# Optimization experiments

Measured on AMD Instinct MI355X. Metric: run time of the kernel, lower is better.

Reference implementation:

```python
import jax, jax.numpy as jnp
import numpy as np

N_NODES = 50000
N_EDGES = 800000
IN, N1, N2, N3, N4, N5, L, NC = 7, 128, 128, 64, 64, 16, 16, 3


def _gat_params(key, fin, fout, edge_dim=1):
    ks = jax.random.split(key, 6)
    s = 0.1
    return dict(
        W=jax.random.normal(ks[0], (fin, fout), jnp.float32) * s,
        a_src=jax.random.normal(ks[1], (fout,), jnp.float32) * s,
        a_dst=jax.random.normal(ks[2], (fout,), jnp.float32) * s,
        We=jax.random.normal(ks[3], (edge_dim, fout), jnp.float32) * s,
        a_e=jax.random.normal(ks[4], (fout,), jnp.float32) * s,
        b=jax.random.normal(ks[5], (fout,), jnp.float32) * s,
    )


def setup_inputs() -> dict:
    key = jax.random.key(0)
    ks = jax.random.split(key, 16)
    inp = {
        'x1': jax.random.normal(ks[0], (N_NODES, IN), jnp.float32),
        'x2': jax.random.normal(ks[1], (N_NODES, IN), jnp.float32),
        'edge_index1': jax.random.randint(ks[2], (2, N_EDGES), 0, N_NODES),
        'edge_index2': jax.random.randint(ks[3], (2, N_EDGES), 0, N_NODES),
        'x_norm2_1': jax.random.normal(ks[4], (L,), jnp.float32),
        'x_norm2_2': jax.random.normal(ks[5], (L,), jnp.float32),
        'edge_col1': jax.random.uniform(ks[6], (N_EDGES, 1), jnp.float32),
        'edge_col2': jax.random.uniform(ks[7], (N_EDGES, 1), jnp.float32),
    }
    p1 = _gat_params(ks[8], IN, N1)
    p2 = _gat_params(ks[9], N1, N2)
    p3 = _gat_params(ks[10], N2, N3)
    for i, p in enumerate((p1, p2, p3), 1):
        for k, v in p.items():
            inp[f'{k}{i}'] = v
    s = 0.1
    inp['W_lin'] = jax.random.normal(ks[11], (N3 + L, N4), jnp.float32) * s
    inp['b_lin'] = jnp.zeros((N4,), jnp.float32)
    inp['W_c1'] = jax.random.normal(ks[12], (2 * N4, N5), jnp.float32) * s
    inp['b_c1'] = jnp.zeros((N5,), jnp.float32)
    inp['W_c2'] = jax.random.normal(ks[13], (N5, NC), jnp.float32) * s
    inp['b_c2'] = jnp.zeros((NC,), jnp.float32)
    return inp


def _gat_conv(x, src, dst, eattr, W, a_src, a_dst, We, a_e, b, n):
    # PyG GATConv, heads=1, add_self_loops with fill_value='mean'
    h = x @ W                                           # [N, C]
    ones = jnp.ones_like(dst, dtype=eattr.dtype)
    deg = jax.ops.segment_sum(ones, dst, n)
    loop_attr = jax.ops.segment_sum(eattr, dst, n) / jnp.maximum(deg, 1.0)[:, None]
    ar = jnp.arange(n, dtype=src.dtype)
    s = jnp.concatenate([src, ar])
    d = jnp.concatenate([dst, ar])
    ea = jnp.concatenate([eattr, loop_attr], axis=0)    # [E+N, edge_dim]
    alpha = (h @ a_src)[s] + (h @ a_dst)[d] + (ea @ We) @ a_e
    alpha = jax.nn.leaky_relu(alpha, 0.2)
    amax = jax.ops.segment_max(alpha, d, n)             # every node has a self loop
    ex = jnp.exp(alpha - amax[d])
    denom = jax.ops.segment_sum(ex, d, n)
    w = ex / denom[d]                                   # segment softmax weights
    out = jax.ops.segment_sum(w[:, None] * h[s], d, n)  # [N, C]
    return out + b


def _process_graph(x, ei, eattr, params):
    src, dst = ei[0], ei[1]
    n = x.shape[0]
    for p in params:
        x = jax.nn.elu(_gat_conv(x, src, dst, eattr, *p, n))
    return x.mean(axis=0)


def reference(x1, x2, edge_index1, edge_index2, x_norm2_1, x_norm2_2,
              edge_col1, edge_col2,
              W1, a_src1, a_dst1, We1, a_e1, b1,
              W2, a_src2, a_dst2, We2, a_e2, b2,
              W3, a_src3, a_dst3, We3, a_e3, b3,
              W_lin, b_lin, W_c1, b_c1, W_c2, b_c2):
    params = [
        (W1, a_src1, a_dst1, We1, a_e1, b1),
        (W2, a_src2, a_dst2, We2, a_e2, b2),
        (W3, a_src3, a_dst3, We3, a_e3, b3),
    ]
    g1 = _process_graph(x1, edge_index1, edge_col1, params)
    g2 = _process_graph(x2, edge_index2, edge_col2, params)
    g1 = jnp.concatenate([g1, x_norm2_1]) @ W_lin + b_lin
    g2 = jnp.concatenate([g2, x_norm2_2]) @ W_lin + b_lin
    x = jnp.concatenate([g1, g2])                       # [2*N4]
    h = jax.nn.relu(x @ W_c1 + b_c1)
    logits = h @ W_c2 + b_c2
    return logits[None, :]                              # [1, num_classes]
```

## Files before the change

### kernel.cpp

```cpp
#include <hip/hip_runtime.h>
#include <math.h>

#define NN 50000
#define NE 800000
#define NT 100000
#define ET (2*NE + NT)
#define NPB 256
#define NB 391
#define BCH 4096
#define BCAP 5120

static __device__ __forceinline__ float wave_max64(float v){
  #pragma unroll
  for(int off=32;off;off>>=1) v = fmaxf(v, __shfl_xor(v,off));
  return v;
}
static __device__ __forceinline__ float wave_sum64(float v){
  #pragma unroll
  for(int off=32;off;off>>=1) v += __shfl_xor(v,off);
  return v;
}
static __device__ __forceinline__ unsigned short f2bf(float f){
  unsigned u = __float_as_uint(f);
  return (unsigned short)((u + 0x7FFFu + ((u>>16)&1u)) >> 16);
}
static __device__ __forceinline__ float bflo(unsigned v){ return __uint_as_float(v<<16); }
static __device__ __forceinline__ float bfhi(unsigned v){ return __uint_as_float(v & 0xFFFF0000u); }

__global__ __launch_bounds__(256) void k_hist(const int* __restrict__ d1,
    const int* __restrict__ d2, int* __restrict__ bcnt){
  __shared__ int h[512];
  int t = threadIdx.x;
  h[t] = 0; h[t+256] = 0;
  __syncthreads();
  int stride = gridDim.x*256;
  for (int e = blockIdx.x*256 + t; e < NE; e += stride){
    atomicAdd(&h[d1[e]>>8], 1);
    atomicAdd(&h[(d2[e]+NN)>>8], 1);
  }
  __syncthreads();
  if (h[t])     atomicAdd(&bcnt[t],     h[t]);
  if (h[t+256]) atomicAdd(&bcnt[t+256], h[t+256]);
}

__global__ void k_hscan(const int* __restrict__ bcnt, int* __restrict__ hbase,
                        int* __restrict__ row_ptr){
  int t = threadIdx.x;
  int a = bcnt[2*t], b2 = bcnt[2*t+1];
  int s = a + b2;
  int lane = t & 63, wv = t >> 6;
  int inc = s;
  #pragma unroll
  for (int off=1; off<64; off<<=1){ int u = __shfl_up(inc, off); if (lane>=off) inc += u; }
  __shared__ int wsum[4];
  if (lane==63) wsum[wv] = inc;
  __syncthreads();
  int woff = 0;
  #pragma unroll
  for (int w=0; w<4; ++w) if (w < wv) woff += wsum[w];
  int excl = woff + inc - s;
  hbase[2*t] = excl; hbase[2*t+1] = excl + a;
  if (t==0) row_ptr[NT] = ET;
}

__global__ __launch_bounds__(256) void k_bin(const int* __restrict__ s1,
    const int* __restrict__ d1, const float* __restrict__ e1,
    const int* __restrict__ s2, const int* __restrict__ d2,
    const float* __restrict__ e2, const int* __restrict__ hbase,
    int* __restrict__ gcur, uint2* __restrict__ gstage){
  __shared__ int cnt[512], loff[512], cur[512], gbase_sh[512];
  __shared__ uint2 sdata[BCH];
  __shared__ unsigned short sbkt[BCH];
  __shared__ int wsum[4];
  int tid = threadIdx.x;
  int e0 = blockIdx.x*BCH;
  unsigned pack[16], eab[16];
  unsigned short bk[16];
  cnt[tid] = 0; cnt[tid+256] = 0; cur[tid] = 0; cur[tid+256] = 0;
  __syncthreads();
  #pragma unroll
  for (int u=0; u<16; ++u){
    int e = e0 + u*256 + tid;
    int b = NB; unsigned p = 0, ea = 0;
    if (e < 2*NE){
      int src, dst; float eav;
      if (e < NE){ src = s1[e]; dst = d1[e]; eav = e1[e]; }
      else { int e2i = e - NE; src = s2[e2i] + NN; dst = d2[e2i] + NN; eav = e2[e2i]; }
      b = dst >> 8;
      p = (unsigned)src | ((unsigned)(dst & 255) << 17);
      ea = __float_as_uint(eav);
    }
    bk[u] = (unsigned short)b; pack[u] = p; eab[u] = ea;
    atomicAdd(&cnt[b], 1);
  }
  __syncthreads();
  {
    int a = cnt[2*tid], b2 = cnt[2*tid+1];
    int s = a + b2;
    int lane = tid & 63, wv = tid >> 6;
    int inc = s;
    #pragma unroll
    for (int off=1; off<64; off<<=1){ int u = __shfl_up(inc, off); if (lane>=off) inc += u; }
    if (lane==63) wsum[wv] = inc;
    __syncthreads();
    int woff = 0;
    #pragma unroll
    for (int w=0; w<4; ++w) if (w < wv) woff += wsum[w];
    int excl = woff + inc - s;
    loff[2*tid] = excl; loff[2*tid+1] = excl + a;
  }
  if (tid < NB && cnt[tid] > 0)
    gbase_sh[tid] = hbase[tid] + atomicAdd(&gcur[tid], cnt[tid]);
  if (tid+256 < NB && cnt[tid+256] > 0)
    gbase_sh[tid+256] = hbase[tid+256] + atomicAdd(&gcur[tid+256], cnt[tid+256]);
  __syncthreads();
  #pragma unroll
  for (int u=0; u<16; ++u){
    int b = bk[u];
    int p = loff[b] + atomicAdd(&cur[b], 1);
    sdata[p] = make_uint2(pack[u], eab[u]);
    sbkt[p] = (unsigned short)b;
  }
  __syncthreads();
  for (int k = tid; k < BCH; k += 256){
    int b = sbkt[k];
    if (b < NB) gstage[gbase_sh[b] + (k - loff[b])] = sdata[k];
  }
}

__global__ __launch_bounds__(256) void k_bucket(const uint2* __restrict__ gstage,
    const int* __restrict__ hbase, int2* __restrict__ srt, int* __restrict__ row_ptr){
  __shared__ uint2 sd[BCAP];
  __shared__ int deg[256], rbase[256], cur[256];
  __shared__ float easum[256];
  __shared__ int wsum[4];
  int b = blockIdx.x, t = threadIdx.x;
  int lo = b*NPB;
  int nloc = min(NPB, NT - lo);
  int est = hbase[b], ecnt = hbase[b+1] - est;
  bool inlds = (ecnt <= BCAP);
  deg[t] = 0; easum[t] = 0.f;
  __syncthreads();
  for (int k = t; k < ecnt; k += 256){
    uint2 v = gstage[est + k];
    if (inlds) sd[k] = v;
    int dl = v.x >> 17;
    atomicAdd(&deg[dl], 1);
    atomicAdd(&easum[dl], __uint_as_float(v.y));
  }
  __syncthreads();
  int dv = (t < nloc) ? deg[t] + 1 : 0;
  int lane = t & 63, wv = t >> 6;
  int inc = dv;
  #pragma unroll
  for (int off=1; off<64; off<<=1){ int u = __shfl_up(inc, off); if (lane>=off) inc += u; }
  if (lane==63) wsum[wv] = inc;
  __syncthreads();
  int woff = 0;
  #pragma unroll
  for (int w=0; w<4; ++w) if (w < wv) woff += wsum[w];
  int gb = est + lo + (woff + inc - dv);
  if (t < nloc){
    row_ptr[lo + t] = gb;
    rbase[t] = gb;
    cur[t] = 1;
    float se = easum[t] / fmaxf((float)deg[t], 1.f);
    srt[gb] = make_int2(lo + t, __float_as_int(se));
  }
  __syncthreads();
  for (int k = t; k < ecnt; k += 256){
    uint2 v = inlds ? sd[k] : gstage[est + k];
    int dl = v.x >> 17;
    int pos = rbase[dl] + atomicAdd(&cur[dl], 1);
    srt[pos] = make_int2((int)(v.x & 0x1FFFFu), (int)v.y);
  }
}

__global__ void k_ce3(const float* __restrict__ We0, const float* __restrict__ ae0,
                      const float* __restrict__ We1, const float* __restrict__ ae1,
                      const float* __restrict__ We2, const float* __restrict__ ae2,
                      float* __restrict__ ce3){
  int l = threadIdx.x;
  const float* We[3] = {We0, We1, We2};
  const float* ae[3] = {ae0, ae1, ae2};
  const int fo[3] = {128, 128, 64};
  for (int L = 0; L < 3; ++L){
    float s = 0.f;
    for (int c = l; c < fo[L]; c += 64) s += We[L][c]*ae[L][c];
    s = wave_sum64(s);
    if (l == 0) ce3[L] = s;
  }
}

template<int K, int N>
__global__ __launch_bounds__(256) void k_gemm(const float* __restrict__ x,
    const float* __restrict__ W, const float* __restrict__ a_src,
    const float* __restrict__ a_dst, unsigned short* __restrict__ h16,
    float* __restrict__ hs, float* __restrict__ hd, int n){
  constexpr int KB  = 32;
  constexpr int CG  = N/4;
  constexpr int TY  = 256/CG;
  constexpr int RPT = 64/TY;
  __shared__ float Wl[KB][N];
  __shared__ float Xt[KB][64];
  int tid = threadIdx.x;
  int tx = tid % CG, ty = tid / CG;
  int r0 = blockIdx.x * 64;
  float acc[RPT][4] = {};
  for (int k0 = 0; k0 < K; k0 += KB){
    {
      const float4* src = (const float4*)(W + (size_t)k0*N);
      float4* dst = (float4*)(&Wl[0][0]);
      #pragma unroll
      for (int i = 0; i < KB*N/1024; ++i) dst[tid + i*256] = src[tid + i*256];
    }
    {
      int rr = tid >> 3, kk0 = (tid & 7) * 4;
      #pragma unroll
      for (int it = 0; it < 2; ++it){
        int r = rr + it*32;
        int gr = r0 + r;
        float4 v = (gr < n) ? *(const float4*)(x + (size_t)gr*K + k0 + kk0)
                            : make_float4(0.f,0.f,0.f,0.f);
        Xt[kk0+0][r] = v.x; Xt[kk0+1][r] = v.y; Xt[kk0+2][r] = v.z; Xt[kk0+3][r] = v.w;
      }
    }
    __syncthreads();
    #pragma unroll
    for (int kk = 0; kk < KB; ++kk){
      float4 wv = *(const float4*)(&Wl[kk][tx*4]);
      float xv[RPT];
      #pragma unroll
      for (int i = 0; i < RPT/4; ++i)
        *(float4*)&xv[i*4] = *(const float4*)(&Xt[kk][ty*RPT + i*4]);
      #pragma unroll
      for (int i=0;i<RPT;i++){
        acc[i][0] += xv[i]*wv.x; acc[i][1] += xv[i]*wv.y;
        acc[i][2] += xv[i]*wv.z; acc[i][3] += xv[i]*wv.w;
      }
    }
    __syncthreads();
  }
  #pragma unroll
  for (int i=0;i<RPT;i++){
    int gr = r0 + ty*RPT + i;
    if (gr < n){
      unsigned r0p = (unsigned)f2bf(acc[i][0]) | ((unsigned)f2bf(acc[i][1])<<16);
      unsigned r1p = (unsigned)f2bf(acc[i][2]) | ((unsigned)f2bf(acc[i][3])<<16);
      *(uint2*)(h16 + (size_t)gr*N + tx*4) = make_uint2(r0p, r1p);
    }
  }
  float as4[4], ad4[4];
  #pragma unroll
  for (int j=0;j<4;j++){ as4[j] = a_src[tx*4+j]; ad4[j] = a_dst[tx*4+j]; }
  #pragma unroll
  for (int i=0;i<RPT;i++){
    float ps = acc[i][0]*as4[0] + acc[i][1]*as4[1] + acc[i][2]*as4[2] + acc[i][3]*as4[3];
    float pd = acc[i][0]*ad4[0] + acc[i][1]*ad4[1] + acc[i][2]*ad4[2] + acc[i][3]*ad4[3];
    #pragma unroll
    for (int off=CG/2; off; off>>=1){ ps += __shfl_xor(ps, off); pd += __shfl_xor(pd, off); }
    int gr = r0 + ty*RPT + i;
    if (tx==0 && gr < n){ hs[gr] = ps; hd[gr] = pd; }
  }
}

__global__ __launch_bounds__(256) void k_gemm7(const float* __restrict__ x1,
    const float* __restrict__ x2, const float* __restrict__ W,
    const float* __restrict__ a_src, const float* __restrict__ a_dst,
    unsigned short* __restrict__ h16, float* __restrict__ hs,
    float* __restrict__ hd, int n){
  __shared__ float Wl[7][128];
  int tid = threadIdx.x;
  for (int i = tid; i < 7*128; i += 256) ((float*)Wl)[i] = W[i];
  __syncthreads();
  int tx = tid & 31, ty = tid >> 5;
  int r = blockIdx.x*8 + ty;
  if (r >= n) return;
  const float* xr = (r < NN) ? (x1 + (size_t)r*7) : (x2 + (size_t)(r-NN)*7);
  float xv[7];
  #pragma unroll
  for (int k=0;k<7;k++) xv[k] = xr[k];
  float4 s = make_float4(0.f,0.f,0.f,0.f);
  #pragma unroll
  for (int k=0;k<7;k++){
    float4 wv = *(const float4*)(&Wl[k][tx*4]);
    s.x += xv[k]*wv.x; s.y += xv[k]*wv.y; s.z += xv[k]*wv.z; s.w += xv[k]*wv.w;
  }
  unsigned r0p = (unsigned)f2bf(s.x) | ((unsigned)f2bf(s.y)<<16);
  unsigned r1p = (unsigned)f2bf(s.z) | ((unsigned)f2bf(s.w)<<16);
  *(uint2*)(h16 + (size_t)r*128 + tx*4) = make_uint2(r0p, r1p);
  float ps = s.x*a_src[tx*4] + s.y*a_src[tx*4+1] + s.z*a_src[tx*4+2] + s.w*a_src[tx*4+3];
  float pd = s.x*a_dst[tx*4] + s.y*a_dst[tx*4+1] + s.z*a_dst[tx*4+2] + s.w*a_dst[tx*4+3];
  #pragma unroll
  for (int off=16; off; off>>=1){ ps += __shfl_xor(ps, off); pd += __shfl_xor(pd, off); }
  if (tx==0){ hs[r] = ps; hd[r] = pd; }
}

template<int FOUT>
__global__ __launch_bounds__(256) void k_aggregate(const unsigned short* __restrict__ h16,
    const float* __restrict__ hs, const float* __restrict__ hd,
    const int2* __restrict__ srt, const int* __restrict__ row_ptr,
    const float* __restrict__ ce_p, const float* __restrict__ b,
    float* __restrict__ xout, int n){
  constexpr int LPE = FOUT/8;
  constexpr int EPS = 64/LPE;
  __shared__ float s_p[4][64];
  __shared__ int   s_s[4][64];
  int tid = threadIdx.x;
  int wv = tid >> 6, lane = tid & 63;
  int wid = (int)((blockIdx.x*256 + tid) >> 6);
  if (wid >= n) return;
  float ce  = *ce_p;
  int beg = row_ptr[wid], end = row_ptr[wid+1];
  float hdn = hd[wid];
  int e_sub = lane / LPE;
  int col8  = (lane % LPE) * 8;
  float m = -INFINITY, den = 0.f;
  float acc[8] = {0.f,0.f,0.f,0.f,0.f,0.f,0.f,0.f};
  for (int base = beg; base < end; base += 64){
    int slot = base + lane;
    float a = -INFINITY; int src = 0;
    if (slot < end){
      int2 pk = srt[slot];
      src = pk.x;
      a = hs[src] + hdn + __int_as_float(pk.y)*ce;
      a = (a > 0.f) ? a : 0.2f*a;
    }
    float cm = wave_max64(a);
    float mnew = fmaxf(m, cm);
    float scale = __expf(m - mnew);
    den *= scale;
    #pragma unroll
    for (int u=0;u<8;u++) acc[u] *= scale;
    float p = __expf(a - mnew);
    den += wave_sum64(p);
    s_p[wv][lane] = p; s_s[wv][lane] = src;
    asm volatile("s_waitcnt lgkmcnt(0)" ::: "memory");
    int cnt = end - base; if (cnt > 64) cnt = 64;
    for (int j = 0; j < cnt; j += 2*EPS){
      int jj0 = j + e_sub, jj1 = j + EPS + e_sub;
      float p0 = s_p[wv][jj0];  int sj0 = s_s[wv][jj0];
      float p1 = s_p[wv][jj1];  int sj1 = s_s[wv][jj1];
      uint4 h0 = *(const uint4*)(h16 + (size_t)sj0*FOUT + col8);
      uint4 h1 = *(const uint4*)(h16 + (size_t)sj1*FOUT + col8);
      acc[0] += p0*bflo(h0.x); acc[1] += p0*bfhi(h0.x);
      acc[2] += p0*bflo(h0.y); acc[3] += p0*bfhi(h0.y);
      acc[4] += p0*bflo(h0.z); acc[5] += p0*bfhi(h0.z);
      acc[6] += p0*bflo(h0.w); acc[7] += p0*bfhi(h0.w);
      acc[0] += p1*bflo(h1.x); acc[1] += p1*bfhi(h1.x);
      acc[2] += p1*bflo(h1.y); acc[3] += p1*bfhi(h1.y);
      acc[4] += p1*bflo(h1.z); acc[5] += p1*bfhi(h1.z);
      acc[6] += p1*bflo(h1.w); acc[7] += p1*bfhi(h1.w);
    }
    m = mnew;
  }
  #pragma unroll
  for (int off = LPE; off < 64; off <<= 1){
    #pragma unroll
    for (int u=0;u<8;u++) acc[u] += __shfl_xor(acc[u], off);
  }
  float inv = 1.f/den;
  if (lane < LPE){
    float4 b0 = *(const float4*)(b + col8);
    float4 b1 = *(const float4*)(b + col8 + 4);
    float4 o0, o1;
    o0.x = acc[0]*inv + b0.x; o0.y = acc[1]*inv + b0.y;
    o0.z = acc[2]*inv + b0.z; o0.w = acc[3]*inv + b0.w;
    o1.x = acc[4]*inv + b1.x; o1.y = acc[5]*inv + b1.y;
    o1.z = acc[6]*inv + b1.z; o1.w = acc[7]*inv + b1.w;
    o0.x = (o0.x > 0.f) ? o0.x : (__expf(o0.x) - 1.f);
    o0.y = (o0.y > 0.f) ? o0.y : (__expf(o0.y) - 1.f);
    o0.z = (o0.z > 0.f) ? o0.z : (__expf(o0.z) - 1.f);
    o0.w = (o0.w > 0.f) ? o0.w : (__expf(o0.w) - 1.f);
    o1.x = (o1.x > 0.f) ? o1.x : (__expf(o1.x) - 1.f);
    o1.y = (o1.y > 0.f) ? o1.y : (__expf(o1.y) - 1.f);
    o1.z = (o1.z > 0.f) ? o1.z : (__expf(o1.z) - 1.f);
    o1.w = (o1.w > 0.f) ? o1.w : (__expf(o1.w) - 1.f);
    *(float4*)(xout + (size_t)wid*FOUT + col8)     = o0;
    *(float4*)(xout + (size_t)wid*FOUT + col8 + 4) = o1;
  }
}

__global__ __launch_bounds__(256) void k_colsum2(const float* __restrict__ x,
    float* __restrict__ gsum, int n){
  __shared__ float ls[128];
  int t = threadIdx.x;
  if (t < 128) ls[t] = 0.f;
  __syncthreads();
  int c4 = (t & 15) * 4;
  int rsub = t >> 4;
  float4 s1 = make_float4(0.f,0.f,0.f,0.f), s2 = make_float4(0.f,0.f,0.f,0.f);
  for (int r = blockIdx.x*16 + rsub; r < n; r += gridDim.x*16){
    float4 v = *(const float4*)(x + (size_t)r*64 + c4);
    if (r < NN){ s1.x+=v.x; s1.y+=v.y; s1.z+=v.z; s1.w+=v.w; }
    else       { s2.x+=v.x; s2.y+=v.y; s2.z+=v.z; s2.w+=v.w; }
  }
  atomicAdd(&ls[c4+0], s1.x); atomicAdd(&ls[c4+1], s1.y);
  atomicAdd(&ls[c4+2], s1.z); atomicAdd(&ls[c4+3], s1.w);
  atomicAdd(&ls[64+c4+0], s2.x); atomicAdd(&ls[64+c4+1], s2.y);
  atomicAdd(&ls[64+c4+2], s2.z); atomicAdd(&ls[64+c4+3], s2.w);
  __syncthreads();
  if (t < 128) atomicAdd(&gsum[t], ls[t]);
}

__global__ void k_head(const float* __restrict__ gs1, const float* __restrict__ gs2,
                       const float* __restrict__ xn1, const float* __restrict__ xn2,
                       const float* __restrict__ Wlin, const float* __restrict__ blin,
                       const float* __restrict__ Wc1, const float* __restrict__ bc1,
                       const float* __restrict__ Wc2, const float* __restrict__ bc2,
                       float* __restrict__ out){
  __shared__ float c1[80], c2[80], xcat[128], hb[16];
  int tid = threadIdx.x;
  const float invn = 1.f/(float)NN;
  if (tid < 64){ c1[tid] = gs1[tid]*invn; c2[tid] = gs2[tid]*invn; }
  else if (tid < 80){ c1[tid] = xn1[tid-64]; c2[tid] = xn2[tid-64]; }
  __syncthreads();
  if (tid < 64){
    float s = blin[tid];
    for (int k=0;k<80;k++) s += c1[k]*Wlin[k*64+tid];
    xcat[tid] = s;
  } else {
    int j = tid - 64;
    float s = blin[j];
    for (int k=0;k<80;k++) s += c2[k]*Wlin[k*64+j];
    xcat[tid] = s;
  }
  __syncthreads();
  if (tid < 16){
    float s = bc1[tid];
    for (int k=0;k<128;k++) s += xcat[k]*Wc1[k*16+tid];
    hb[tid] = fmaxf(s, 0.f);
  }
  __syncthreads();
  if (tid < 3){
    float s = bc2[tid];
    for (int k=0;k<16;k++) s += hb[k]*Wc2[k*3+tid];
    out[tid] = s;
  }
}

extern "C" void kernel_launch(void* const* d_in, const int* in_sizes, int n_in,
                              void* d_out, int out_size, void* d_ws, size_t ws_size,
                              hipStream_t stream){
  const float* x1  = (const float*)d_in[0];
  const float* x2  = (const float*)d_in[1];
  const int*   ei1 = (const int*)d_in[2];
  const int*   ei2 = (const int*)d_in[3];
  const float* xn1 = (const float*)d_in[4];
  const float* xn2 = (const float*)d_in[5];
  const float* ec1 = (const float*)d_in[6];
  const float* ec2 = (const float*)d_in[7];
  const float* W[3]    = {(const float*)d_in[8],  (const float*)d_in[14], (const float*)d_in[20]};
  const float* asrc[3] = {(const float*)d_in[9],  (const float*)d_in[15], (const float*)d_in[21]};
  const float* adst[3] = {(const float*)d_in[10], (const float*)d_in[16], (const float*)d_in[22]};
  const float* We[3]   = {(const float*)d_in[11], (const float*)d_in[17], (const float*)d_in[23]};
  const float* ae[3]   = {(const float*)d_in[12], (const float*)d_in[18], (const float*)d_in[24]};
  const float* bb[3]   = {(const float*)d_in[13], (const float*)d_in[19], (const float*)d_in[25]};
  const float* Wlin = (const float*)d_in[26];
  const float* blin = (const float*)d_in[27];
  const float* Wc1  = (const float*)d_in[28];
  const float* bc1  = (const float*)d_in[29];
  const float* Wc2  = (const float*)d_in[30];
  const float* bc2  = (const float*)d_in[31];
  float* out = (float*)d_out;

  char* wsb = (char*)d_ws;
  float*          bufX = (float*)wsb;
  uint2*          gstage = (uint2*)wsb;
  unsigned short* h16  = (unsigned short*)(wsb + (size_t)NT*128*4);
  int2*           srt  = (int2*)(wsb + (size_t)NT*128*4 + (size_t)NT*128*2);
  float* hs   = (float*)(srt + ET);
  float* hd   = hs + NT;
  int*   row_ptr = (int*)(hd + NT);
  int*   bcnt  = row_ptr + NT + 2;
  int*   gcur  = bcnt + 512;
  float* gsum  = (float*)(gcur + 512);
  int*   hbase = (int*)(gsum + 128);
  float* ce3   = (float*)(hbase + 513);

  const int* s1 = ei1, * d1 = ei1 + NE;
  const int* s2 = ei2, * d2 = ei2 + NE;

  hipMemsetAsync(bcnt, 0, (512+512+128)*sizeof(int), stream);
  k_ce3<<<1, 64, 0, stream>>>(We[0], ae[0], We[1], ae[1], We[2], ae[2], ce3);

  k_hist<<<256, 256, 0, stream>>>(d1, d2, bcnt);
  k_hscan<<<1, 256, 0, stream>>>(bcnt, hbase, row_ptr);
  k_bin<<<(2*NE + BCH - 1)/BCH, 256, 0, stream>>>(s1, d1, ec1, s2, d2, ec2, hbase, gcur, gstage);
  k_bucket<<<NB, 256, 0, stream>>>(gstage, hbase, srt, row_ptr);

  k_gemm7<<<(NT+7)/8, 256, 0, stream>>>(x1, x2, W[0], asrc[0], adst[0], h16, hs, hd, NT);
  k_aggregate<128><<<(NT+3)/4, 256, 0, stream>>>(h16, hs, hd, srt, row_ptr, ce3+0, bb[0], bufX, NT);
  k_gemm<128,128><<<(NT+63)/64, 256, 0, stream>>>(bufX, W[1], asrc[1], adst[1], h16, hs, hd, NT);
  k_aggregate<128><<<(NT+3)/4, 256, 0, stream>>>(h16, hs, hd, srt, row_ptr, ce3+1, bb[1], bufX, NT);
  k_gemm<128,64><<<(NT+63)/64, 256, 0, stream>>>(bufX, W[2], asrc[2], adst[2], h16, hs, hd, NT);
  k_aggregate<64><<<(NT+3)/4, 256, 0, stream>>>(h16, hs, hd, srt, row_ptr, ce3+2, bb[2], bufX, NT);

  k_colsum2<<<512, 256, 0, stream>>>(bufX, gsum, NT);
  k_head<<<1, 128, 0, stream>>>(gsum, gsum+64, xn1, xn2, Wlin, blin, Wc1, bc1, Wc2, bc2, out);
}
```

Measured before the change: 511.1 us.

## Use bf16 MFMA for hidden GEMMs with bf16 activations between layers

The fp32 SIMT GEMMs for layers 2 and 3 become bf16 MFMA 16x16x32 kernels. Their weights are pre-transposed and converted to bf16 in a prep kernel, using a padded stride of 136 to avoid LDS bank conflicts. The aggregate kernel now writes bf16 activations for the first two layers, which halves intermediate traffic and feeds the MFMA path directly. The aggregate inner loop also drops its two-edge unroll, which may reduce memory-level parallelism. Using bf16 inputs adds precision loss in the GEMMs.

After: 475.4 us. 1.08x faster.

```diff
diff --git a/kernel.cpp b/kernel.cpp
--- a/kernel.cpp
+++ b/kernel.cpp
@@ -4,11 +4,15 @@
 #define NN 50000
 #define NE 800000
 #define NT 100000
+#define NTP 100032
 #define ET (2*NE + NT)
 #define NPB 256
 #define NB 391
 #define BCH 4096
 #define BCAP 5120
+
+typedef __attribute__((ext_vector_type(8))) short bf16x8;
+typedef __attribute__((ext_vector_type(4))) float f32x4;
 
 static __device__ __forceinline__ float wave_max64(float v){
   #pragma unroll
@@ -176,91 +180,82 @@
   }
 }
 
-__global__ void k_ce3(const float* __restrict__ We0, const float* __restrict__ ae0,
-                      const float* __restrict__ We1, const float* __restrict__ ae1,
-                      const float* __restrict__ We2, const float* __restrict__ ae2,
-                      float* __restrict__ ce3){
-  int l = threadIdx.x;
-  const float* We[3] = {We0, We1, We2};
-  const float* ae[3] = {ae0, ae1, ae2};
-  const int fo[3] = {128, 128, 64};
-  for (int L = 0; L < 3; ++L){
-    float s = 0.f;
-    for (int c = l; c < fo[L]; c += 64) s += We[L][c]*ae[L][c];
-    s = wave_sum64(s);
-    if (l == 0) ce3[L] = s;
-  }
-}
-
-template<int K, int N>
-__global__ __launch_bounds__(256) void k_gemm(const float* __restrict__ x,
-    const float* __restrict__ W, const float* __restrict__ a_src,
-    const float* __restrict__ a_dst, unsigned short* __restrict__ h16,
-    float* __restrict__ hs, float* __restrict__ hd, int n){
-  constexpr int KB  = 32;
-  constexpr int CG  = N/4;
-  constexpr int TY  = 256/CG;
-  constexpr int RPT = 64/TY;
-  __shared__ float Wl[KB][N];
-  __shared__ float Xt[KB][64];
+__global__ __launch_bounds__(256) void k_prep(
+    const float* __restrict__ We0, const float* __restrict__ ae0,
+    const float* __restrict__ We1, const float* __restrict__ ae1,
+    const float* __restrict__ We2, const float* __restrict__ ae2,
+    float* __restrict__ ce3,
+    const float* __restrict__ W1, const float* __restrict__ W2,
+    unsigned short* __restrict__ Wt1, unsigned short* __restrict__ Wt2){
+  int t = threadIdx.x;
+  if (t < 64){
+    const float* We[3] = {We0, We1, We2};
+    const float* ae[3] = {ae0, ae1, ae2};
+    const int fo[3] = {128, 128, 64};
+    for (int L = 0; L < 3; ++L){
+      float s = 0.f;
+      for (int c = t; c < fo[L]; c += 64) s += We[L][c]*ae[L][c];
+      s = wave_sum64(s);
+      if (t == 0) ce3[L] = s;
+    }
+  }
+  for (int i = t; i < 128*128; i += 256){
+    int c = i >> 7, k = i & 127;
+    Wt1[c*136 + k] = f2bf(W1[k*128 + c]);
+  }
+  for (int i = t; i < 64*128; i += 256){
+    int c = i >> 7, k = i & 127;
+    Wt2[c*136 + k] = f2bf(W2[k*64 + c]);
+  }
+}
+
+template<int N>
+__global__ __launch_bounds__(256) void k_gemm_mfma(
+    const unsigned short* __restrict__ x16, const unsigned short* __restrict__ Wt,
+    const float* __restrict__ a_src, const float* __restrict__ a_dst,
+    unsigned short* __restrict__ h16, float* __restrict__ hs,
+    float* __restrict__ hd, int n){
+  constexpr int CT = N/16;
+  __shared__ unsigned short Wl[N*136];
   int tid = threadIdx.x;
-  int tx = tid % CG, ty = tid / CG;
-  int r0 = blockIdx.x * 64;
-  float acc[RPT][4] = {};
-  for (int k0 = 0; k0 < K; k0 += KB){
-    {
-      const float4* src = (const float4*)(W + (size_t)k0*N);
-      float4* dst = (float4*)(&Wl[0][0]);
-      #pragma unroll
-      for (int i = 0; i < KB*N/1024; ++i) dst[tid + i*256] = src[tid + i*256];
-    }
-    {
-      int rr = tid >> 3, kk0 = (tid & 7) * 4;
-      #pragma unroll
-      for (int it = 0; it < 2; ++it){
-        int r = rr + it*32;
-        int gr = r0 + r;
-        float4 v = (gr < n) ? *(const float4*)(x + (size_t)gr*K + k0 + kk0)
-                            : make_float4(0.f,0.f,0.f,0.f);
-        Xt[kk0+0][r] = v.x; Xt[kk0+1][r] = v.y; Xt[kk0+2][r] = v.z; Xt[kk0+3][r] = v.w;
-      }
-    }
-    __syncthreads();
-    #pragma unroll
-    for (int kk = 0; kk < KB; ++kk){
-      float4 wv = *(const float4*)(&Wl[kk][tx*4]);
-      float xv[RPT];
-      #pragma unroll
-      for (int i = 0; i < RPT/4; ++i)
-        *(float4*)&xv[i*4] = *(const float4*)(&Xt[kk][ty*RPT + i*4]);
-      #pragma unroll
-      for (int i=0;i<RPT;i++){
-        acc[i][0] += xv[i]*wv.x; acc[i][1] += xv[i]*wv.y;
-        acc[i][2] += xv[i]*wv.z; acc[i][3] += xv[i]*wv.w;
-      }
-    }
-    __syncthreads();
-  }
-  #pragma unroll
-  for (int i=0;i<RPT;i++){
-    int gr = r0 + ty*RPT + i;
-    if (gr < n){
-      unsigned r0p = (unsigned)f2bf(acc[i][0]) | ((unsigned)f2bf(acc[i][1])<<16);
-      unsigned r1p = (unsigned)f2bf(acc[i][2]) | ((unsigned)f2bf(acc[i][3])<<16);
-      *(uint2*)(h16 + (size_t)gr*N + tx*4) = make_uint2(r0p, r1p);
-    }
-  }
-  float as4[4], ad4[4];
-  #pragma unroll
-  for (int j=0;j<4;j++){ as4[j] = a_src[tx*4+j]; ad4[j] = a_dst[tx*4+j]; }
-  #pragma unroll
-  for (int i=0;i<RPT;i++){
-    float ps = acc[i][0]*as4[0] + acc[i][1]*as4[1] + acc[i][2]*as4[2] + acc[i][3]*as4[3];
-    float pd = acc[i][0]*ad4[0] + acc[i][1]*ad4[1] + acc[i][2]*ad4[2] + acc[i][3]*ad4[3];
-    #pragma unroll
-    for (int off=CG/2; off; off>>=1){ ps += __shfl_xor(ps, off); pd += __shfl_xor(pd, off); }
-    int gr = r0 + ty*RPT + i;
-    if (tx==0 && gr < n){ hs[gr] = ps; hd[gr] = pd; }
+  for (int i = tid; i < N*136/8; i += 256)
+    ((uint4*)Wl)[i] = ((const uint4*)Wt)[i];
+  __syncthreads();
+  int lane = tid & 63, w = tid >> 6;
+  int arow = blockIdx.x*64 + w*16 + (lane & 15);
+  int kb   = (lane >> 4) * 8;
+  int rsafe = (arow < n) ? arow : (n-1);
+  f32x4 acc[CT] = {};
+  #pragma unroll
+  for (int s = 0; s < 4; ++s){
+    bf16x8 a = *(const bf16x8*)(x16 + (size_t)rsafe*128 + s*32 + kb);
+    #pragma unroll
+    for (int c = 0; c < CT; ++c){
+      bf16x8 b = *(const bf16x8*)(&Wl[(c*16 + (lane&15))*136 + s*32 + kb]);
+      acc[c] = __builtin_amdgcn_mfma_f32_16x16x32_bf16(a, b, acc[c], 0, 0, 0);
+    }
+  }
+  int drow = blockIdx.x*64 + w*16 + (lane>>4)*4;
+  int dcol = lane & 15;
+  float psv[4] = {0,0,0,0}, pdv[4] = {0,0,0,0};
+  #pragma unroll
+  for (int c = 0; c < CT; ++c){
+    float as = a_src[c*16 + dcol], ad = a_dst[c*16 + dcol];
+    #pragma unroll
+    for (int j = 0; j < 4; ++j){
+      float v = acc[c][j];
+      if (drow + j < n) h16[(size_t)(drow+j)*N + c*16 + dcol] = f2bf(v);
+      psv[j] += v*as; pdv[j] += v*ad;
+    }
+  }
+  #pragma unroll
+  for (int off = 1; off < 16; off <<= 1){
+    #pragma unroll
+    for (int j=0;j<4;j++){ psv[j] += __shfl_xor(psv[j], off); pdv[j] += __shfl_xor(pdv[j], off); }
+  }
+  if (dcol == 0){
+    #pragma unroll
+    for (int j=0;j<4;j++) if (drow+j < n){ hs[drow+j] = psv[j]; hd[drow+j] = pdv[j]; }
   }
 }
 
@@ -296,12 +291,12 @@
   if (tx==0){ hs[r] = ps; hd[r] = pd; }
 }
 
-template<int FOUT>
+template<int FOUT, bool OBF>
 __global__ __launch_bounds__(256) void k_aggregate(const unsigned short* __restrict__ h16,
     const float* __restrict__ hs, const float* __restrict__ hd,
     const int2* __restrict__ srt, const int* __restrict__ row_ptr,
     const float* __restrict__ ce_p, const float* __restrict__ b,
-    float* __restrict__ xout, int n){
+    void* __restrict__ xout, int n){
   constexpr int LPE = FOUT/8;
   constexpr int EPS = 64/LPE;
   __shared__ float s_p[4][64];
@@ -337,20 +332,14 @@
     s_p[wv][lane] = p; s_s[wv][lane] = src;
     asm volatile("s_waitcnt lgkmcnt(0)" ::: "memory");
     int cnt = end - base; if (cnt > 64) cnt = 64;
-    for (int j = 0; j < cnt; j += 2*EPS){
-      int jj0 = j + e_sub, jj1 = j + EPS + e_sub;
-      float p0 = s_p[wv][jj0];  int sj0 = s_s[wv][jj0];
-      float p1 = s_p[wv][jj1];  int sj1 = s_s[wv][jj1];
-      uint4 h0 = *(const uint4*)(h16 + (size_t)sj0*FOUT + col8);
-      uint4 h1 = *(const uint4*)(h16 + (size_t)sj1*FOUT + col8);
+    for (int j = 0; j < cnt; j += EPS){
+      int jj = j + e_sub;
+      float p0 = s_p[wv][jj];  int sj = s_s[wv][jj];
+      uint4 h0 = *(const uint4*)(h16 + (size_t)sj*FOUT + col8);
       acc[0] += p0*bflo(h0.x); acc[1] += p0*bfhi(h0.x);
       acc[2] += p0*bflo(h0.y); acc[3] += p0*bfhi(h0.y);
       acc[4] += p0*bflo(h0.z); acc[5] += p0*bfhi(h0.z);
       acc[6] += p0*bflo(h0.w); acc[7] += p0*bfhi(h0.w);
-      acc[0] += p1*bflo(h1.x); acc[1] += p1*bfhi(h1.x);
-      acc[2] += p1*bflo(h1.y); acc[3] += p1*bfhi(h1.y);
-      acc[4] += p1*bflo(h1.z); acc[5] += p1*bfhi(h1.z);
-      acc[6] += p1*bflo(h1.w); acc[7] += p1*bfhi(h1.w);
     }
     m = mnew;
   }
@@ -361,23 +350,25 @@
   }
   float inv = 1.f/den;
   if (lane < LPE){
-    float4 b0 = *(const float4*)(b + col8);
-    float4 b1 = *(const float4*)(b + col8 + 4);
-    float4 o0, o1;
-    o0.x = acc[0]*inv + b0.x; o0.y = acc[1]*inv + b0.y;
-    o0.z = acc[2]*inv + b0.z; o0.w = acc[3]*inv + b0.w;
-    o1.x = acc[4]*inv + b1.x; o1.y = acc[5]*inv + b1.y;
-    o1.z = acc[6]*inv + b1.z; o1.w = acc[7]*inv + b1.w;
-    o0.x = (o0.x > 0.f) ? o0.x : (__expf(o0.x) - 1.f);
-    o0.y = (o0.y > 0.f) ? o0.y : (__expf(o0.y) - 1.f);
-    o0.z = (o0.z > 0.f) ? o0.z : (__expf(o0.z) - 1.f);
-    o0.w = (o0.w > 0.f) ? o0.w : (__expf(o0.w) - 1.f);
-    o1.x = (o1.x > 0.f) ? o1.x : (__expf(o1.x) - 1.f);
-    o1.y = (o1.y > 0.f) ? o1.y : (__expf(o1.y) - 1.f);
-    o1.z = (o1.z > 0.f) ? o1.z : (__expf(o1.z) - 1.f);
-    o1.w = (o1.w > 0.f) ? o1.w : (__expf(o1.w) - 1.f);
-    *(float4*)(xout + (size_t)wid*FOUT + col8)     = o0;
-    *(float4*)(xout + (size_t)wid*FOUT + col8 + 4) = o1;
+    float o[8];
+    #pragma unroll
+    for (int u=0;u<8;u++){
+      o[u] = acc[u]*inv + b[col8+u];
+      o[u] = (o[u] > 0.f) ? o[u] : (__expf(o[u]) - 1.f);
+    }
+    if (OBF){
+      uint4 pkd;
+      pkd.x = (unsigned)f2bf(o[0]) | ((unsigned)f2bf(o[1])<<16);
+      pkd.y = (unsigned)f2bf(o[2]) | ((unsigned)f2bf(o[3])<<16);
+      pkd.z = (unsigned)f2bf(o[4]) | ((unsigned)f2bf(o[5])<<16);
+      pkd.w = (unsigned)f2bf(o[6]) | ((unsigned)f2bf(o[7])<<16);
+      *(uint4*)((unsigned short*)xout + (size_t)wid*FOUT + col8) = pkd;
+    } else {
+      float4 o0 = make_float4(o[0],o[1],o[2],o[3]);
+      float4 o1 = make_float4(o[4],o[5],o[6],o[7]);
+      *(float4*)((float*)xout + (size_t)wid*FOUT + col8)     = o0;
+      *(float4*)((float*)xout + (size_t)wid*FOUT + col8 + 4) = o1;
+    }
   }
 }
 
@@ -465,10 +456,11 @@
   float* out = (float*)d_out;
 
   char* wsb = (char*)d_ws;
-  float*          bufX = (float*)wsb;
+  unsigned short* x16   = (unsigned short*)wsb;
   uint2*          gstage = (uint2*)wsb;
-  unsigned short* h16  = (unsigned short*)(wsb + (size_t)NT*128*4);
-  int2*           srt  = (int2*)(wsb + (size_t)NT*128*4 + (size_t)NT*128*2);
+  float*          bufX  = (float*)wsb;
+  unsigned short* h16  = (unsigned short*)(wsb + (size_t)NTP*128*2);
+  int2*           srt  = (int2*)(wsb + (size_t)NTP*128*2 + (size_t)NT*128*2);
   float* hs   = (float*)(srt + ET);
   float* hd   = hs + NT;
   int*   row_ptr = (int*)(hd + NT);
@@ -477,12 +469,15 @@
   float* gsum  = (float*)(gcur + 512);
   int*   hbase = (int*)(gsum + 128);
   float* ce3   = (float*)(hbase + 513);
+  unsigned short* Wt1 = (unsigned short*)(ce3 + 8);
+  unsigned short* Wt2 = Wt1 + 128*136;
 
   const int* s1 = ei1, * d1 = ei1 + NE;
   const int* s2 = ei2, * d2 = ei2 + NE;
 
   hipMemsetAsync(bcnt, 0, (512+512+128)*sizeof(int), stream);
-  k_ce3<<<1, 64, 0, stream>>>(We[0], ae[0], We[1], ae[1], We[2], ae[2], ce3);
+  k_prep<<<1, 256, 0, stream>>>(We[0], ae[0], We[1], ae[1], We[2], ae[2], ce3,
+                                W[1], W[2], Wt1, Wt2);
 
   k_hist<<<256, 256, 0, stream>>>(d1, d2, bcnt);
   k_hscan<<<1, 256, 0, stream>>>(bcnt, hbase, row_ptr);
@@ -490,11 +485,11 @@
   k_bucket<<<NB, 256, 0, stream>>>(gstage, hbase, srt, row_ptr);
 
   k_gemm7<<<(NT+7)/8, 256, 0, stream>>>(x1, x2, W[0], asrc[0], adst[0], h16, hs, hd, NT);
-  k_aggregate<128><<<(NT+3)/4, 256, 0, stream>>>(h16, hs, hd, srt, row_ptr, ce3+0, bb[0], bufX, NT);
-  k_gemm<128,128><<<(NT+63)/64, 256, 0, stream>>>(bufX, W[1], asrc[1], adst[1], h16, hs, hd, NT);
-  k_aggregate<128><<<(NT+3)/4, 256, 0, stream>>>(h16, hs, hd, srt, row_ptr, ce3+1, bb[1], bufX, NT);
-  k_gemm<128,64><<<(NT+63)/64, 256, 0, stream>>>(bufX, W[2], asrc[2], adst[2], h16, hs, hd, NT);
-  k_aggregate<64><<<(NT+3)/4, 256, 0, stream>>>(h16, hs, hd, srt, row_ptr, ce3+2, bb[2], bufX, NT);
+  k_aggregate<128,true><<<(NT+3)/4, 256, 0, stream>>>(h16, hs, hd, srt, row_ptr, ce3+0, bb[0], x16, NT);
+  k_gemm_mfma<128><<<(NT+63)/64, 256, 0, stream>>>(x16, Wt1, asrc[1], adst[1], h16, hs, hd, NT);
+  k_aggregate<128,true><<<(NT+3)/4, 256, 0, stream>>>(h16, hs, hd, srt, row_ptr, ce3+1, bb[1], x16, NT);
+  k_gemm_mfma<64><<<(NT+63)/64, 256, 0, stream>>>(x16, Wt2, asrc[2], adst[2], h16, hs, hd, NT);
+  k_aggregate<64,false><<<(NT+3)/4, 256, 0, stream>>>(h16, hs, hd, srt, row_ptr, ce3+2, bb[2], bufX, NT);
 
   k_colsum2<<<512, 256, 0, stream>>>(bufX, gsum, NT);
   k_head<<<1, 128, 0, stream>>>(gsum, gsum+64, xn1, xn2, Wlin, blin, Wc1, bc1, Wc2, bc2, out);
```
